# Kernel optimization log

Hardware: AMD Instinct MI355X
Metric: run time of the kernel (lower is better)

## Reference

```python
import jax, jax.numpy as jnp
import numpy as np

PATCH_DIM = 256
TRANS_DIM = 256
K_PATCH = 8


def _gelu(x):
    return jax.nn.gelu(x, approximate=False)  # torch nn.GELU default is exact


def setup_inputs() -> dict:
    key = jax.random.key(0)
    ks = jax.random.split(key, 20)
    s = 0.02
    d, t = PATCH_DIM, TRANS_DIM
    return {
        "x": jax.random.normal(ks[0], (4, 4096, 3 + d), dtype=jnp.float32),
        # weights stored (in, out): y = x @ W + b  (equiv to torch Linear)
        "W_in": jax.random.normal(ks[1], (d, t), jnp.float32) * s,
        "b_in": jax.random.normal(ks[2], (t,), jnp.float32) * s,
        "Wq": jax.random.normal(ks[3], (t, t), jnp.float32) * s,
        "Wk": jax.random.normal(ks[4], (t, t), jnp.float32) * s,
        "Wv": jax.random.normal(ks[5], (t, t), jnp.float32) * s,
        "Wg1": jax.random.normal(ks[6], (t, t), jnp.float32) * s,
        "bg1": jax.random.normal(ks[7], (t,), jnp.float32) * s,
        "Wg2": jax.random.normal(ks[8], (t, t), jnp.float32) * s,
        "bg2": jax.random.normal(ks[9], (t,), jnp.float32) * s,
        "W_out": jax.random.normal(ks[10], (t, d), jnp.float32) * s,
        "b_out": jax.random.normal(ks[11], (d,), jnp.float32) * s,
        "Wp1": jax.random.normal(ks[12], (10, 128), jnp.float32) * s,
        "bp1": jax.random.normal(ks[13], (128,), jnp.float32) * s,
        "Wp2": jax.random.normal(ks[14], (128, t), jnp.float32) * s,
        "bp2": jax.random.normal(ks[15], (t,), jnp.float32) * s,
    }


def reference(x, W_in, b_in, Wq, Wk, Wv, Wg1, bg1, Wg2, bg2, W_out, b_out, Wp1, bp1, Wp2, bp2):
    centroid = x[:, :, :3]              # [B,S,3]
    pre = x[:, :, 3:]                   # [B,S,D]
    B, S, _ = centroid.shape
    scale = TRANS_DIM ** (-0.5)

    # square_distance: ||a-b||^2 = |a|^2 + |b|^2 - 2 a.b
    sq = jnp.sum(centroid * centroid, axis=-1)                     # [B,S]
    dist = sq[:, :, None] + sq[:, None, :] - 2.0 * jnp.einsum(
        "bsd,btd->bst", centroid, centroid)                        # [B,S,S]
    idx = jnp.argsort(dist, axis=-1)[:, :, :K_PATCH]               # [B,S,k]

    # index_points gather: [B,S,k,3]
    knn = jax.vmap(lambda c, i: c[i])(centroid, idx)
    ref_vec = knn - centroid[:, :, None, :]
    pos_struct = jnp.concatenate([
        jnp.broadcast_to(centroid[:, :, None, :], (B, S, K_PATCH, 3)),
        knn,
        ref_vec,
        jnp.linalg.norm(ref_vec, axis=-1, keepdims=True),
    ], axis=-1)                                                    # [B,S,k,10]

    pos_h = _gelu(pos_struct @ Wp1 + bp1) @ Wp2 + bp2              # [B,S,k,T]
    pos_emb = jnp.max(pos_h, axis=2)                               # [B,S,T]

    h = pre @ W_in + b_in + pos_emb                                # [B,S,T]
    q, k, v = h @ Wq, h @ Wk, h @ Wv
    attn = (_gelu((q - k) @ Wg1 + bg1) @ Wg2 + bg2) * scale
    attn = jax.nn.softmax(attn, axis=-1)                           # over feature dim
    res = attn * v
    return res @ W_out + b_out + pre                               # [B,S,D]
```

## Files before the change

kernel.cpp:

```cpp
#include <hip/hip_runtime.h>
#include <hip/hip_bf16.h>
#include <math.h>

#define S_   4096
#define XROW 259

typedef const float* fpp;
typedef __attribute__((ext_vector_type(8))) short   s8b;
typedef __attribute__((ext_vector_type(4))) float   f32x4;

__device__ __forceinline__ float us2f(unsigned short u){ return __uint_as_float(((unsigned)u)<<16); }
__device__ __forceinline__ unsigned short f2bu(float f){
  __hip_bfloat16 h = __float2bfloat16(f);
  return *reinterpret_cast<unsigned short*>(&h);
}
__device__ __forceinline__ float gelu_f(float v){
  float u2 = 2.0f * v * fmaf(0.0356774081f, v*v, 0.7978845608f);
  float e  = __expf(u2);
  return v * (1.0f - __builtin_amdgcn_rcpf(e + 1.0f));
}

__global__ __launch_bounds__(256) void k_prep(
    fpp W_in, fpp Wq, fpp Wk, fpp Wv, fpp Wg1, fpp Wg2, fpp W_out, fpp Wp2, fpp Wp1,
    fpp x, unsigned short* __restrict__ FO, float4* __restrict__ cbuf)
{
  int bb = blockIdx.x, wv = threadIdx.x>>6, lane = threadIdx.x&63;
  if (bb < 192) {
    int m  = bb >> 5;
    int fi = (bb & 31)*4 + wv;
    int c = fi >> 3, s = fi & 7;
    int col = c*16 + (lane&15);
    int k0  = s*32 + (lane>>4)*8;
    fpp Wm = (m==0)?W_in:(m==2)?Wv:(m==3)?Wg1:(m==4)?Wg2:(m==5)?W_out:Wq;
    s8b v;
#pragma unroll
    for (int j=0;j<8;j++){
      float f = Wm[(size_t)(k0+j)*256 + col];
      if (m==1) f -= Wk[(size_t)(k0+j)*256 + col];
      v[j] = (short)f2bu(f);
    }
    *(s8b*)(FO + (size_t)m*65536 + (size_t)fi*512 + lane*8) = v;
  } else if (bb < 208) {
    int fi = (bb-192)*4 + wv;
    int c = fi >> 2, s = fi & 3;
    int col = c*16 + (lane&15);
    int k0  = s*32 + (lane>>4)*8;
    s8b v;
#pragma unroll
    for (int j=0;j<8;j++) v[j] = (short)f2bu(Wp2[(size_t)(k0+j)*256 + col]);
    *(s8b*)(FO + 393216 + (size_t)fi*512 + lane*8) = v;
  } else if (bb < 210) {
    int fi = (bb-208)*4 + wv;
    int col = fi*16 + (lane&15);
    int k0  = (lane>>4)*8;
    s8b v;
#pragma unroll
    for (int j=0;j<8;j++){
      int k = k0 + j;
      v[j] = (k < 10) ? (short)f2bu(Wp1[(size_t)k*128 + col]) : (short)0;
    }
    *(s8b*)(FO + 425984 + (size_t)fi*512 + lane*8) = v;
  } else {
    int t = (bb-210)*256 + threadIdx.x;
    size_t xrow = (size_t)t * XROW;
    float cx = x[xrow], cy = x[xrow+1], cz = x[xrow+2];
    cbuf[t] = make_float4(cx, cy, cz, 0.5f*fmaf(cz,cz,fmaf(cy,cy,cx*cx)));
  }
}

__global__ __launch_bounds__(512,4) void k_knn(const float4* __restrict__ cbuf,
                                               unsigned short* __restrict__ idxw)
{
  __shared__ float4 cent4[S_];
  const int rowbase = blockIdx.x * 32;
  const int b = rowbase >> 12;
  const float4* cb = cbuf + (size_t)b*S_;
  for (int t = threadIdx.x; t < S_; t += 512) cent4[t] = cb[t];
  __syncthreads();
  const int r = threadIdx.x >> 4;
  const int L = threadIdx.x & 15;
  const int s = (rowbase & (S_-1)) + r;
  float4 cs = cent4[s];
  const float nsx = -cs.x, nsy = -cs.y, nsz = -cs.z;
  unsigned bk0=0xFFFFFFFFu, bk1=0xFFFFFFFFu, bk2=0xFFFFFFFFu, bk3=0xFFFFFFFFu;
  int t = L;
#pragma unroll 4
  for (int i = 0; i < 256; ++i) {
    float4 c = cent4[t];
    float m = fmaf(nsx, c.x, fmaf(nsy, c.y, fmaf(nsz, c.z, c.w)));
    unsigned ub = __float_as_uint(m);
    ub ^= ((unsigned)((int)ub >> 31)) | 0x80000000u;
    unsigned kk = (ub & 0xFFFFF000u) | (unsigned)t;
    unsigned lo;
    lo = min(kk,bk0); kk = max(kk,bk0); bk0 = lo;
    lo = min(kk,bk1); kk = max(kk,bk1); bk1 = lo;
    lo = min(kk,bk2); kk = max(kk,bk2); bk2 = lo;
    bk3 = min(kk,bk3);
    t += 16;
  }
  size_t obase = (size_t)(rowbase + r) * 8;
  int h = 0;
#pragma unroll
  for (int round = 0; round < 8; ++round) {
    unsigned mdv = (h==0)?bk0:(h==1)?bk1:(h==2)?bk2:(h==3)?bk3:0xFFFFFFFFu;
    unsigned gd = mdv;
#pragma unroll
    for (int off=1; off<16; off<<=1)
      gd = min(gd, (unsigned)__shfl_xor((int)gd, off));
    if (L == 0) idxw[obase + round] = (unsigned short)(gd & 0xFFFu);
    h += (mdv == gd) ? 1 : 0;
  }
}

__global__ __launch_bounds__(512,4) void k_mega(
    fpp x, const unsigned short* __restrict__ idxw,
    fpp bp1, fpp bp2,
    const unsigned short* __restrict__ FO,
    fpp b_in, fpp bg1, fpp bg2, fpp b_out,
    float* __restrict__ out)
{
  __shared__ __align__(16) char pool[50688];
  __shared__ __align__(16) unsigned short pe[8448];
  unsigned short* X0 = (unsigned short*)pool;
  unsigned short* X1 = X0 + 8448;
  unsigned short* X2 = X1 + 8448;
  unsigned short (*psb)[40]  = (unsigned short (*)[40])pool;
  unsigned short (*hh)[136]  = (unsigned short (*)[136])(pool + 20480);

  const int tid = threadIdx.x, lane = tid & 63, wv = tid >> 6;
  const int arow = lane & 15, akb = lane >> 4, rbase = akb*4;
  const int ctb = wv*2;
  const int tok0 = blockIdx.x * 32, b = tok0 >> 12;
  const unsigned short* FO2 = FO + 393216;
  const unsigned short* FO3 = FO + 425984;
  const int col0 = ctb*16 + arow, col1 = col0 + 16;

  s8b bf3 = *(const s8b*)(FO3 + wv*512 + lane*8);
  float b1v = bp1[wv*16 + arow];
  float bp2v0 = bp2[col0], bp2v1 = bp2[col1];

  if (tid < 256) {
    int tk = tid >> 3;
    size_t grow = (size_t)(tok0 + tk), xrow = grow * XROW;
    float cx=x[xrow], cy=x[xrow+1], cz=x[xrow+2];
    int nb = idxw[grow*8 + (tid & 7)];
    size_t nrow = ((size_t)(b*S_ + nb)) * XROW;
    float nx=x[nrow], ny=x[nrow+1], nz=x[nrow+2];
    float rx=nx-cx, ry=ny-cy, rz=nz-cz;
    float nrm = sqrtf(fmaf(rz,rz,fmaf(ry,ry,rx*rx)));
    unsigned short* p = psb[tid];
    s8b v0 = { (short)f2bu(cx),(short)f2bu(cy),(short)f2bu(cz),(short)f2bu(nx),
               (short)f2bu(ny),(short)f2bu(nz),(short)f2bu(rx),(short)f2bu(ry) };
    s8b v1 = { (short)f2bu(rz),(short)f2bu(nrm),0,0,0,0,0,0 };
    s8b vz = { 0,0,0,0,0,0,0,0 };
    *(s8b*)(p) = v0; *(s8b*)(p+8) = v1; *(s8b*)(p+16) = vz; *(s8b*)(p+24) = vz;
  }
  __syncthreads();

  for (int c=0;c<4;++c){
    f32x4 h4[4];
#pragma unroll
    for (int rt=0;rt<4;++rt){
      s8b af = *(const s8b*)(&psb[c*64 + rt*16 + arow][akb*8]);
      h4[rt] = __builtin_amdgcn_mfma_f32_16x16x32_bf16(af, bf3, (f32x4){0.f,0.f,0.f,0.f}, 0,0,0);
    }
#pragma unroll
    for (int rt=0;rt<4;++rt)
#pragma unroll
      for (int rr=0;rr<4;++rr)
        hh[rt*16 + rbase + rr][wv*16 + arow] = f2bu(gelu_f(h4[rt][rr] + b1v));
    __syncthreads();
    f32x4 a2c[4][2];
#pragma unroll
    for (int rt=0;rt<4;++rt){ a2c[rt][0]=(f32x4){0.f,0.f,0.f,0.f}; a2c[rt][1]=(f32x4){0.f,0.f,0.f,0.f}; }
#pragma unroll
    for (int s=0;s<4;++s){
      s8b af0 = *(const s8b*)(&hh[ 0 + arow][s*32 + akb*8]);
      s8b af1 = *(const s8b*)(&hh[16 + arow][s*32 + akb*8]);
      s8b af2 = *(const s8b*)(&hh[32 + arow][s*32 + akb*8]);
      s8b af3v= *(const s8b*)(&hh[48 + arow][s*32 + akb*8]);
#pragma unroll
      for (int i=0;i<2;++i){
        s8b bf = *(const s8b*)(FO2 + ((size_t)((ctb+i)*4 + s))*512 + lane*8);
        a2c[0][i] = __builtin_amdgcn_mfma_f32_16x16x32_bf16(af0,  bf, a2c[0][i], 0,0,0);
        a2c[1][i] = __builtin_amdgcn_mfma_f32_16x16x32_bf16(af1,  bf, a2c[1][i], 0,0,0);
        a2c[2][i] = __builtin_amdgcn_mfma_f32_16x16x32_bf16(af2,  bf, a2c[2][i], 0,0,0);
        a2c[3][i] = __builtin_amdgcn_mfma_f32_16x16x32_bf16(af3v, bf, a2c[3][i], 0,0,0);
      }
    }
#pragma unroll
    for (int rt=0;rt<4;++rt)
#pragma unroll
      for (int i=0;i<2;++i){
        float pm = fmaxf(fmaxf(a2c[rt][i][0],a2c[rt][i][1]), fmaxf(a2c[rt][i][2],a2c[rt][i][3]));
        pm = fmaxf(pm, __shfl_xor(pm, 16));
        if ((akb & 1) == 0)
          pe[(c*8 + rt*2 + (akb>>1))*264 + (ctb+i)*16 + arow] = f2bu(pm + (i ? bp2v1 : bp2v0));
      }
    __syncthreads();
  }

#pragma unroll
  for (int p=0;p<2;++p){
    int i2 = p*512 + tid;
    int row = i2 >> 5, cb2 = i2 & 31;
    const float* src = x + (size_t)(tok0 + row)*XROW + 3 + cb2*8;
    s8b v;
#pragma unroll
    for (int j=0;j<8;j++) v[j] = (short)f2bu(src[j]);
    *(s8b*)(X0 + row*264 + cb2*8) = v;
  }
  __syncthreads();

  f32x4 acc[2][2];
  auto gphase = [&](const unsigned short* A, const unsigned short* FOm){
#pragma unroll
    for (int rt=0;rt<2;++rt){ acc[rt][0]=(f32x4){0.f,0.f,0.f,0.f}; acc[rt][1]=(f32x4){0.f,0.f,0.f,0.f}; }
#pragma unroll
    for (int s=0;s<8;++s){
      s8b a0 = *(const s8b*)(A + arow*264 + s*32 + akb*8);
      s8b a1 = *(const s8b*)(A + (16+arow)*264 + s*32 + akb*8);
#pragma unroll
      for (int i=0;i<2;++i){
        s8b bf = *(const s8b*)(FOm + ((size_t)((ctb+i)*8 + s))*512 + lane*8);
        acc[0][i] = __builtin_amdgcn_mfma_f32_16x16x32_bf16(a0, bf, acc[0][i], 0,0,0);
        acc[1][i] = __builtin_amdgcn_mfma_f32_16x16x32_bf16(a1, bf, acc[1][i], 0,0,0);
      }
    }
  };

  gphase(X0, FO);
#pragma unroll
  for (int i=0;i<2;++i){
    int col = i ? col1 : col0;
    float bi = b_in[col];
#pragma unroll
    for (int rt=0;rt<2;++rt)
#pragma unroll
      for (int rr=0;rr<4;++rr){
        int row = rt*16 + rbase + rr;
        X1[row*264 + col] = f2bu(acc[rt][i][rr] + bi + us2f(pe[row*264 + col]));
      }
  }
  __syncthreads();

  gphase(X1, FO + 65536);
#pragma unroll
  for (int i=0;i<2;++i){
    int col = i ? col1 : col0;
#pragma unroll
    for (int rt=0;rt<2;++rt)
#pragma unroll
      for (int rr=0;rr<4;++rr)
        X0[(rt*16 + rbase + rr)*264 + col] = f2bu(acc[rt][i][rr]);
  }
  __syncthreads();

  gphase(X0, FO + 196608);
#pragma unroll
  for (int i=0;i<2;++i){
    int col = i ? col1 : col0;
    float bi = bg1[col];
#pragma unroll
    for (int rt=0;rt<2;++rt)
#pragma unroll
      for (int rr=0;rr<4;++rr)
        X2[(rt*16 + rbase + rr)*264 + col] = f2bu(gelu_f(acc[rt][i][rr] + bi));
  }
  __syncthreads();

  gphase(X2, FO + 262144);
#pragma unroll
  for (int i=0;i<2;++i){
    int col = i ? col1 : col0;
    float bi = bg2[col];
#pragma unroll
    for (int rt=0;rt<2;++rt)
#pragma unroll
      for (int rr=0;rr<4;++rr)
        X0[(rt*16 + rbase + rr)*264 + col] = f2bu((acc[rt][i][rr] + bi) * 0.0625f);
  }
  __syncthreads();

  {
    int row = tid >> 4, li = tid & 15;
    unsigned short* rp = X0 + row*264 + li*16;
    uint4 u0 = *(uint4*)rp, u1 = *(uint4*)(rp + 8);
    float f[16];
    f[0]=us2f(u0.x&0xffff); f[1]=us2f(u0.x>>16); f[2]=us2f(u0.y&0xffff); f[3]=us2f(u0.y>>16);
    f[4]=us2f(u0.z&0xffff); f[5]=us2f(u0.z>>16); f[6]=us2f(u0.w&0xffff); f[7]=us2f(u0.w>>16);
    f[8]=us2f(u1.x&0xffff); f[9]=us2f(u1.x>>16); f[10]=us2f(u1.y&0xffff); f[11]=us2f(u1.y>>16);
    f[12]=us2f(u1.z&0xffff); f[13]=us2f(u1.z>>16); f[14]=us2f(u1.w&0xffff); f[15]=us2f(u1.w>>16);
    float mx = f[0];
#pragma unroll
    for (int i=1;i<16;i++) mx = fmaxf(mx, f[i]);
#pragma unroll
    for (int o=1;o<16;o<<=1) mx = fmaxf(mx, __shfl_xor(mx, o));
    float ssum = 0.f;
#pragma unroll
    for (int i=0;i<16;i++){ f[i] = __expf(f[i]-mx); ssum += f[i]; }
#pragma unroll
    for (int o=1;o<16;o<<=1) ssum += __shfl_xor(ssum, o);
    float inv = __builtin_amdgcn_rcpf(ssum);
    uint4 w0, w1;
    w0.x=f2bu(f[0]*inv) | ((unsigned)f2bu(f[1]*inv)<<16);
    w0.y=f2bu(f[2]*inv) | ((unsigned)f2bu(f[3]*inv)<<16);
    w0.z=f2bu(f[4]*inv) | ((unsigned)f2bu(f[5]*inv)<<16);
    w0.w=f2bu(f[6]*inv) | ((unsigned)f2bu(f[7]*inv)<<16);
    w1.x=f2bu(f[8]*inv) | ((unsigned)f2bu(f[9]*inv)<<16);
    w1.y=f2bu(f[10]*inv)| ((unsigned)f2bu(f[11]*inv)<<16);
    w1.z=f2bu(f[12]*inv)| ((unsigned)f2bu(f[13]*inv)<<16);
    w1.w=f2bu(f[14]*inv)| ((unsigned)f2bu(f[15]*inv)<<16);
    *(uint4*)rp = w0; *(uint4*)(rp+8) = w1;
  }
  __syncthreads();

  gphase(X1, FO + 131072);
#pragma unroll
  for (int i=0;i<2;++i){
    int col = i ? col1 : col0;
#pragma unroll
    for (int rt=0;rt<2;++rt)
#pragma unroll
      for (int rr=0;rr<4;++rr){
        int row = rt*16 + rbase + rr;
        X2[row*264 + col] = f2bu(us2f(X0[row*264 + col]) * acc[rt][i][rr]);
      }
  }
  __syncthreads();

  gphase(X2, FO + 327680);
#pragma unroll
  for (int i=0;i<2;++i){
    int col = i ? col1 : col0;
    float bo = b_out[col];
#pragma unroll
    for (int rt=0;rt<2;++rt)
#pragma unroll
      for (int rr=0;rr<4;++rr){
        size_t row = (size_t)(tok0 + rt*16 + rbase + rr);
        out[row*256 + col] = acc[rt][i][rr] + bo + x[row*XROW + 3 + col];
      }
  }
}

extern "C" void kernel_launch(void* const* d_in, const int* in_sizes, int n_in,
                              void* d_out, int out_size, void* d_ws, size_t ws_size,
                              hipStream_t stream)
{
  fpp x    = (fpp)d_in[0];
  fpp W_in = (fpp)d_in[1];  fpp b_in = (fpp)d_in[2];
  fpp Wq   = (fpp)d_in[3];  fpp Wk   = (fpp)d_in[4];  fpp Wv = (fpp)d_in[5];
  fpp Wg1  = (fpp)d_in[6];  fpp bg1  = (fpp)d_in[7];
  fpp Wg2  = (fpp)d_in[8];  fpp bg2  = (fpp)d_in[9];
  fpp W_out= (fpp)d_in[10]; fpp b_out= (fpp)d_in[11];
  fpp Wp1  = (fpp)d_in[12]; fpp bp1  = (fpp)d_in[13];
  fpp Wp2  = (fpp)d_in[14]; fpp bp2  = (fpp)d_in[15];

  char* ws = (char*)d_ws;
  unsigned short* idxw = (unsigned short*)ws;
  unsigned short* FO   = (unsigned short*)(ws + 262144);

  float4* cbuf = (float4*)((char*)d_out + 16515072);

  k_prep<<<274, 256, 0, stream>>>(W_in,Wq,Wk,Wv,Wg1,Wg2,W_out,Wp2,Wp1, x, FO, cbuf);
  k_knn <<<512, 512, 0, stream>>>(cbuf, idxw);
  k_mega<<<512, 512, 0, stream>>>(x, idxw, bp1, bp2, FO,
                                  b_in, bg1, bg2, b_out, (float*)d_out);
}
```

Measured before the change: 76.13 us.

## Halve tokens per block in mega kernel to double grid size

```diff
diff --git a/kernel.cpp b/kernel.cpp
--- a/kernel.cpp
+++ b/kernel.cpp
@@ -119,18 +119,18 @@
     fpp b_in, fpp bg1, fpp bg2, fpp b_out,
     float* __restrict__ out)
 {
-  __shared__ __align__(16) char pool[50688];
-  __shared__ __align__(16) unsigned short pe[8448];
-  unsigned short* X0 = (unsigned short*)pool;
-  unsigned short* X1 = X0 + 8448;
-  unsigned short* X2 = X1 + 8448;
-  unsigned short (*psb)[40]  = (unsigned short (*)[40])pool;
-  unsigned short (*hh)[136]  = (unsigned short (*)[136])(pool + 20480);
+  __shared__ __align__(16) char pool[36096];
+  unsigned short* psb = (unsigned short*)pool;
+  unsigned short* hh  = (unsigned short*)(pool + 10240);
+  unsigned short* X0  = (unsigned short*)pool;
+  unsigned short* X1  = (unsigned short*)(pool + 8448);
+  unsigned short* X2  = (unsigned short*)(pool + 16896);
+  unsigned short* pe  = (unsigned short*)(pool + 27648);
 
   const int tid = threadIdx.x, lane = tid & 63, wv = tid >> 6;
   const int arow = lane & 15, akb = lane >> 4, rbase = akb*4;
   const int ctb = wv*2;
-  const int tok0 = blockIdx.x * 32, b = tok0 >> 12;
+  const int tok0 = blockIdx.x * 16, b = tok0 >> 12;
   const unsigned short* FO2 = FO + 393216;
   const unsigned short* FO3 = FO + 425984;
   const int col0 = ctb*16 + arow, col1 = col0 + 16;
@@ -139,7 +139,7 @@
   float b1v = bp1[wv*16 + arow];
   float bp2v0 = bp2[col0], bp2v1 = bp2[col1];
 
-  if (tid < 256) {
+  if (tid < 128) {
     int tk = tid >> 3;
     size_t grow = (size_t)(tok0 + tk), xrow = grow * XROW;
     float cx=x[xrow], cy=x[xrow+1], cz=x[xrow+2];
@@ -148,7 +148,7 @@
     float nx=x[nrow], ny=x[nrow+1], nz=x[nrow+2];
     float rx=nx-cx, ry=ny-cy, rz=nz-cz;
     float nrm = sqrtf(fmaf(rz,rz,fmaf(ry,ry,rx*rx)));
-    unsigned short* p = psb[tid];
+    unsigned short* p = psb + tid*40;
     s8b v0 = { (short)f2bu(cx),(short)f2bu(cy),(short)f2bu(cz),(short)f2bu(nx),
                (short)f2bu(ny),(short)f2bu(nz),(short)f2bu(rx),(short)f2bu(ry) };
     s8b v1 = { (short)f2bu(rz),(short)f2bu(nrm),0,0,0,0,0,0 };
@@ -157,53 +157,50 @@
   }
   __syncthreads();
 
-  for (int c=0;c<4;++c){
+  for (int c=0;c<2;++c){
     f32x4 h4[4];
 #pragma unroll
     for (int rt=0;rt<4;++rt){
-      s8b af = *(const s8b*)(&psb[c*64 + rt*16 + arow][akb*8]);
+      s8b af = *(const s8b*)(psb + (c*64 + rt*16 + arow)*40 + akb*8);
       h4[rt] = __builtin_amdgcn_mfma_f32_16x16x32_bf16(af, bf3, (f32x4){0.f,0.f,0.f,0.f}, 0,0,0);
     }
 #pragma unroll
     for (int rt=0;rt<4;++rt)
 #pragma unroll
       for (int rr=0;rr<4;++rr)
-        hh[rt*16 + rbase + rr][wv*16 + arow] = f2bu(gelu_f(h4[rt][rr] + b1v));
+        hh[(rt*16 + rbase + rr)*136 + wv*16 + arow] = f2bu(gelu_f(h4[rt][rr] + b1v));
     __syncthreads();
-    f32x4 a2c[4][2];
-#pragma unroll
-    for (int rt=0;rt<4;++rt){ a2c[rt][0]=(f32x4){0.f,0.f,0.f,0.f}; a2c[rt][1]=(f32x4){0.f,0.f,0.f,0.f}; }
-#pragma unroll
-    for (int s=0;s<4;++s){
-      s8b af0 = *(const s8b*)(&hh[ 0 + arow][s*32 + akb*8]);
-      s8b af1 = *(const s8b*)(&hh[16 + arow][s*32 + akb*8]);
-      s8b af2 = *(const s8b*)(&hh[32 + arow][s*32 + akb*8]);
-      s8b af3v= *(const s8b*)(&hh[48 + arow][s*32 + akb*8]);
-#pragma unroll
-      for (int i=0;i<2;++i){
-        s8b bf = *(const s8b*)(FO2 + ((size_t)((ctb+i)*4 + s))*512 + lane*8);
-        a2c[0][i] = __builtin_amdgcn_mfma_f32_16x16x32_bf16(af0,  bf, a2c[0][i], 0,0,0);
-        a2c[1][i] = __builtin_amdgcn_mfma_f32_16x16x32_bf16(af1,  bf, a2c[1][i], 0,0,0);
-        a2c[2][i] = __builtin_amdgcn_mfma_f32_16x16x32_bf16(af2,  bf, a2c[2][i], 0,0,0);
-        a2c[3][i] = __builtin_amdgcn_mfma_f32_16x16x32_bf16(af3v, bf, a2c[3][i], 0,0,0);
+#pragma unroll
+    for (int p=0;p<2;++p){
+      f32x4 a2c[2][2];
+#pragma unroll
+      for (int rt=0;rt<2;++rt){ a2c[rt][0]=(f32x4){0.f,0.f,0.f,0.f}; a2c[rt][1]=(f32x4){0.f,0.f,0.f,0.f}; }
+#pragma unroll
+      for (int s=0;s<4;++s){
+        s8b ah0 = *(const s8b*)(hh + (p*32 +      arow)*136 + s*32 + akb*8);
+        s8b ah1 = *(const s8b*)(hh + (p*32 + 16 + arow)*136 + s*32 + akb*8);
+#pragma unroll
+        for (int i=0;i<2;++i){
+          s8b bf = *(const s8b*)(FO2 + ((size_t)((ctb+i)*4 + s))*512 + lane*8);
+          a2c[0][i] = __builtin_amdgcn_mfma_f32_16x16x32_bf16(ah0, bf, a2c[0][i], 0,0,0);
+          a2c[1][i] = __builtin_amdgcn_mfma_f32_16x16x32_bf16(ah1, bf, a2c[1][i], 0,0,0);
+        }
       }
-    }
-#pragma unroll
-    for (int rt=0;rt<4;++rt)
-#pragma unroll
-      for (int i=0;i<2;++i){
-        float pm = fmaxf(fmaxf(a2c[rt][i][0],a2c[rt][i][1]), fmaxf(a2c[rt][i][2],a2c[rt][i][3]));
-        pm = fmaxf(pm, __shfl_xor(pm, 16));
-        if ((akb & 1) == 0)
-          pe[(c*8 + rt*2 + (akb>>1))*264 + (ctb+i)*16 + arow] = f2bu(pm + (i ? bp2v1 : bp2v0));
-      }
+#pragma unroll
+      for (int rt=0;rt<2;++rt)
+#pragma unroll
+        for (int i=0;i<2;++i){
+          float pm = fmaxf(fmaxf(a2c[rt][i][0],a2c[rt][i][1]), fmaxf(a2c[rt][i][2],a2c[rt][i][3]));
+          pm = fmaxf(pm, __shfl_xor(pm, 16));
+          if ((akb & 1) == 0)
+            pe[(c*8 + p*4 + rt*2 + (akb>>1))*264 + (ctb+i)*16 + arow] = f2bu(pm + (i ? bp2v1 : bp2v0));
+        }
+    }
     __syncthreads();
   }
 
-#pragma unroll
-  for (int p=0;p<2;++p){
-    int i2 = p*512 + tid;
-    int row = i2 >> 5, cb2 = i2 & 31;
+  {
+    int row = tid >> 5, cb2 = tid & 31;
     const float* src = x + (size_t)(tok0 + row)*XROW + 3 + cb2*8;
     s8b v;
 #pragma unroll
@@ -212,19 +209,16 @@
   }
   __syncthreads();
 
-  f32x4 acc[2][2];
+  f32x4 acc[2];
   auto gphase = [&](const unsigned short* A, const unsigned short* FOm){
-#pragma unroll
-    for (int rt=0;rt<2;++rt){ acc[rt][0]=(f32x4){0.f,0.f,0.f,0.f}; acc[rt][1]=(f32x4){0.f,0.f,0.f,0.f}; }
+    acc[0]=(f32x4){0.f,0.f,0.f,0.f}; acc[1]=(f32x4){0.f,0.f,0.f,0.f};
 #pragma unroll
     for (int s=0;s<8;++s){
       s8b a0 = *(const s8b*)(A + arow*264 + s*32 + akb*8);
-      s8b a1 = *(const s8b*)(A + (16+arow)*264 + s*32 + akb*8);
 #pragma unroll
       for (int i=0;i<2;++i){
         s8b bf = *(const s8b*)(FOm + ((size_t)((ctb+i)*8 + s))*512 + lane*8);
-        acc[0][i] = __builtin_amdgcn_mfma_f32_16x16x32_bf16(a0, bf, acc[0][i], 0,0,0);
-        acc[1][i] = __builtin_amdgcn_mfma_f32_16x16x32_bf16(a1, bf, acc[1][i], 0,0,0);
+        acc[i] = __builtin_amdgcn_mfma_f32_16x16x32_bf16(a0, bf, acc[i], 0,0,0);
       }
     }
   };
@@ -235,12 +229,10 @@
     int col = i ? col1 : col0;
     float bi = b_in[col];
 #pragma unroll
-    for (int rt=0;rt<2;++rt)
-#pragma unroll
-      for (int rr=0;rr<4;++rr){
-        int row = rt*16 + rbase + rr;
-        X1[row*264 + col] = f2bu(acc[rt][i][rr] + bi + us2f(pe[row*264 + col]));
-      }
+    for (int rr=0;rr<4;++rr){
+      int row = rbase + rr;
+      X1[row*264 + col] = f2bu(acc[i][rr] + bi + us2f(pe[row*264 + col]));
+    }
   }
   __syncthreads();
 
@@ -249,10 +241,8 @@
   for (int i=0;i<2;++i){
     int col = i ? col1 : col0;
 #pragma unroll
-    for (int rt=0;rt<2;++rt)
-#pragma unroll
-      for (int rr=0;rr<4;++rr)
-        X0[(rt*16 + rbase + rr)*264 + col] = f2bu(acc[rt][i][rr]);
+    for (int rr=0;rr<4;++rr)
+      X0[(rbase + rr)*264 + col] = f2bu(acc[i][rr]);
   }
   __syncthreads();
 
@@ -262,10 +252,8 @@
     int col = i ? col1 : col0;
     float bi = bg1[col];
 #pragma unroll
-    for (int rt=0;rt<2;++rt)
-#pragma unroll
-      for (int rr=0;rr<4;++rr)
-        X2[(rt*16 + rbase + rr)*264 + col] = f2bu(gelu_f(acc[rt][i][rr] + bi));
+    for (int rr=0;rr<4;++rr)
+      X2[(rbase + rr)*264 + col] = f2bu(gelu_f(acc[i][rr] + bi));
   }
   __syncthreads();
 
@@ -275,43 +263,32 @@
     int col = i ? col1 : col0;
     float bi = bg2[col];
 #pragma unroll
-    for (int rt=0;rt<2;++rt)
-#pragma unroll
-      for (int rr=0;rr<4;++rr)
-        X0[(rt*16 + rbase + rr)*264 + col] = f2bu((acc[rt][i][rr] + bi) * 0.0625f);
+    for (int rr=0;rr<4;++rr)
+      X0[(rbase + rr)*264 + col] = f2bu((acc[i][rr] + bi) * 0.0625f);
   }
   __syncthreads();
 
   {
-    int row = tid >> 4, li = tid & 15;
-    unsigned short* rp = X0 + row*264 + li*16;
-    uint4 u0 = *(uint4*)rp, u1 = *(uint4*)(rp + 8);
-    float f[16];
-    f[0]=us2f(u0.x&0xffff); f[1]=us2f(u0.x>>16); f[2]=us2f(u0.y&0xffff); f[3]=us2f(u0.y>>16);
-    f[4]=us2f(u0.z&0xffff); f[5]=us2f(u0.z>>16); f[6]=us2f(u0.w&0xffff); f[7]=us2f(u0.w>>16);
-    f[8]=us2f(u1.x&0xffff); f[9]=us2f(u1.x>>16); f[10]=us2f(u1.y&0xffff); f[11]=us2f(u1.y>>16);
-    f[12]=us2f(u1.z&0xffff); f[13]=us2f(u1.z>>16); f[14]=us2f(u1.w&0xffff); f[15]=us2f(u1.w>>16);
+    int row = tid >> 5, li = tid & 31;
+    unsigned short* rp = X0 + row*264 + li*8;
+    s8b v0 = *(const s8b*)rp;
+    float f[8];
+#pragma unroll
+    for (int j=0;j<8;++j) f[j] = us2f((unsigned short)v0[j]);
     float mx = f[0];
 #pragma unroll
-    for (int i=1;i<16;i++) mx = fmaxf(mx, f[i]);
-#pragma unroll
-    for (int o=1;o<16;o<<=1) mx = fmaxf(mx, __shfl_xor(mx, o));
+    for (int i=1;i<8;i++) mx = fmaxf(mx, f[i]);
+#pragma unroll
+    for (int o=1;o<32;o<<=1) mx = fmaxf(mx, __shfl_xor(mx, o));
     float ssum = 0.f;
 #pragma unroll
-    for (int i=0;i<16;i++){ f[i] = __expf(f[i]-mx); ssum += f[i]; }
-#pragma unroll
-    for (int o=1;o<16;o<<=1) ssum += __shfl_xor(ssum, o);
+    for (int i=0;i<8;i++){ f[i] = __expf(f[i]-mx); ssum += f[i]; }
+#pragma unroll
+    for (int o=1;o<32;o<<=1) ssum += __shfl_xor(ssum, o);
     float inv = __builtin_amdgcn_rcpf(ssum);
-    uint4 w0, w1;
-    w0.x=f2bu(f[0]*inv) | ((unsigned)f2bu(f[1]*inv)<<16);
-    w0.y=f2bu(f[2]*inv) | ((unsigned)f2bu(f[3]*inv)<<16);
-    w0.z=f2bu(f[4]*inv) | ((unsigned)f2bu(f[5]*inv)<<16);
-    w0.w=f2bu(f[6]*inv) | ((unsigned)f2bu(f[7]*inv)<<16);
-    w1.x=f2bu(f[8]*inv) | ((unsigned)f2bu(f[9]*inv)<<16);
-    w1.y=f2bu(f[10]*inv)| ((unsigned)f2bu(f[11]*inv)<<16);
-    w1.z=f2bu(f[12]*inv)| ((unsigned)f2bu(f[13]*inv)<<16);
-    w1.w=f2bu(f[14]*inv)| ((unsigned)f2bu(f[15]*inv)<<16);
-    *(uint4*)rp = w0; *(uint4*)(rp+8) = w1;
+#pragma unroll
+    for (int j=0;j<8;++j) v0[j] = (short)f2bu(f[j]*inv);
+    *(s8b*)rp = v0;
   }
   __syncthreads();
 
@@ -320,12 +297,10 @@
   for (int i=0;i<2;++i){
     int col = i ? col1 : col0;
 #pragma unroll
-    for (int rt=0;rt<2;++rt)
-#pragma unroll
-      for (int rr=0;rr<4;++rr){
-        int row = rt*16 + rbase + rr;
-        X2[row*264 + col] = f2bu(us2f(X0[row*264 + col]) * acc[rt][i][rr]);
-      }
+    for (int rr=0;rr<4;++rr){
+      int row = rbase + rr;
+      X2[row*264 + col] = f2bu(us2f(X0[row*264 + col]) * acc[i][rr]);
+    }
   }
   __syncthreads();
 
@@ -335,12 +310,10 @@
     int col = i ? col1 : col0;
     float bo = b_out[col];
 #pragma unroll
-    for (int rt=0;rt<2;++rt)
-#pragma unroll
-      for (int rr=0;rr<4;++rr){
-        size_t row = (size_t)(tok0 + rt*16 + rbase + rr);
-        out[row*256 + col] = acc[rt][i][rr] + bo + x[row*XROW + 3 + col];
-      }
+    for (int rr=0;rr<4;++rr){
+      size_t row = (size_t)(tok0 + rbase + rr);
+      out[row*256 + col] = acc[i][rr] + bo + x[row*XROW + 3 + col];
+    }
   }
 }
 
@@ -365,6 +338,6 @@
 
   k_prep<<<274, 256, 0, stream>>>(W_in,Wq,Wk,Wv,Wg1,Wg2,W_out,Wp2,Wp1, x, FO, cbuf);
   k_knn <<<512, 512, 0, stream>>>(cbuf, idxw);
-  k_mega<<<512, 512, 0, stream>>>(x, idxw, bp1, bp2, FO,
+  k_mega<<<1024,512, 0, stream>>>(x, idxw, bp1, bp2, FO,
                                   b_in, bg1, bg2, b_out, (float*)d_out);
 }
```

Measured after the change: 86.83 us. 1.14x slower.
